# Kernel optimization log

Measured on AMD Instinct MI355X. Metric: run time of the kernel, lower is better.

## Reference

```python
import jax, jax.numpy as jnp
import numpy as np

N, E, B = 50000, 800000, 512
IN, H, OUT = 128, 64, 32
BN_EPS = 1e-5


def setup_inputs() -> dict:
    key = jax.random.key(0)
    ks = jax.random.split(key, 32)
    inp = {}
    inp["x"] = jax.random.normal(ks[0], (N, IN), dtype=jnp.float32)
    inp["edge_index"] = jax.random.randint(ks[1], (2, E), 0, N, dtype=jnp.int64)
    inp["batch"] = jnp.sort(jax.random.randint(ks[2], (N,), 0, B, dtype=jnp.int64))
    inp["batch_size"] = B
    # GINConv MLP params: Linear(cin,H) -> BN(H) -> ReLU -> Linear(H,H)
    cins = [IN, H, H]
    ki = 3
    for i, cin in enumerate(cins):
        inp[f"c{i}_W1"] = jax.random.normal(ks[ki], (cin, H), dtype=jnp.float32) / np.sqrt(cin); ki += 1
        inp[f"c{i}_b1"] = jnp.zeros((H,), jnp.float32)
        inp[f"c{i}_g1"] = jnp.ones((H,), jnp.float32)
        inp[f"c{i}_bt1"] = jnp.zeros((H,), jnp.float32)
        inp[f"c{i}_W2"] = jax.random.normal(ks[ki], (H, H), dtype=jnp.float32) / np.sqrt(H); ki += 1
        inp[f"c{i}_b2"] = jnp.zeros((H,), jnp.float32)
    # final MLP (norm=None): Linear(H,H) -> ReLU -> [dropout, eval: identity] -> Linear(H,OUT)
    inp["f_W1"] = jax.random.normal(ks[ki], (H, H), dtype=jnp.float32) / np.sqrt(H); ki += 1
    inp["f_b1"] = jnp.zeros((H,), jnp.float32)
    inp["f_W2"] = jax.random.normal(ks[ki], (H, OUT), dtype=jnp.float32) / np.sqrt(H)
    inp["f_b2"] = jnp.zeros((OUT,), jnp.float32)
    return inp


def _bn(h, g, bt):
    # BatchNorm1d, training-mode statistics (biased variance), eps=1e-5
    mean = h.mean(axis=0)
    var = ((h - mean) ** 2).mean(axis=0)
    return g * (h - mean) * jax.lax.rsqrt(var + BN_EPS) + bt


def _gin_conv(x, src, dst, W1, b1, g1, bt1, W2, b2):
    # sum-aggregate neighbor features: agg[i] = sum_{(j->i)} x[j]
    agg = jax.ops.segment_sum(x[src], dst, num_segments=N)  # [N,H_in]
    h = x + agg  # (1+eps)*x + agg, eps=0
    h = jax.nn.relu(_bn(h @ W1 + b1, g1, bt1))
    return h @ W2 + b2


def reference(x, edge_index, batch, batch_size,
              c0_W1, c0_b1, c0_g1, c0_bt1, c0_W2, c0_b2,
              c1_W1, c1_b1, c1_g1, c1_bt1, c1_W2, c1_b2,
              c2_W1, c2_b1, c2_g1, c2_bt1, c2_W2, c2_b2,
              f_W1, f_b1, f_W2, f_b2):
    src, dst = edge_index[0], edge_index[1]
    convs = [(c0_W1, c0_b1, c0_g1, c0_bt1, c0_W2, c0_b2),
             (c1_W1, c1_b1, c1_g1, c1_bt1, c1_W2, c1_b2),
             (c2_W1, c2_b1, c2_g1, c2_bt1, c2_W2, c2_b2)]
    for p in convs:
        x = jax.nn.relu(_gin_conv(x, src, dst, *p))
    # global_add_pool over graph ids
    pooled = jax.ops.segment_sum(x, batch, num_segments=batch_size)  # [B,H]
    h = jax.nn.relu(pooled @ f_W1 + f_b1)  # dropout=0.5 skipped (eval mode)
    return h @ f_W2 + f_b2  # [B,OUT]
```

## Files before the change

### kernel.cpp

```cpp
#include <hip/hip_runtime.h>
#include <hip/hip_bf16.h>

#define NN 50000
#define EE 800000
#define BB 512
#define DIN 128
#define HH 64
#define DOUT 32
#define BN_EPS 1e-5f
#define SCAN_BLOCKS 196

template <int CIN>
__global__ __launch_bounds__(256) void proj_kernel(const float* __restrict__ X,
                                                   const float* __restrict__ W,
                                                   float* __restrict__ Q)
{
    __shared__ float sW[CIN * 64];
    __shared__ float sX[16 * CIN];
    const int tid = threadIdx.x;
    const int row0 = blockIdx.x * 16;

    for (int i = tid; i < CIN * 16; i += 256)
        ((float4*)sW)[i] = ((const float4*)W)[i];
    const float* Xb = X + (size_t)row0 * CIN;
    for (int i = tid; i < 16 * CIN / 4; i += 256)
        ((float4*)sX)[i] = ((const float4*)Xb)[i];
    __syncthreads();

    const int col = tid & 63;
    const int r0  = tid >> 6;
    float acc[4] = {0.f, 0.f, 0.f, 0.f};
    for (int k = 0; k < CIN; k += 4) {
        const float w0 = sW[(k + 0) * 64 + col];
        const float w1 = sW[(k + 1) * 64 + col];
        const float w2 = sW[(k + 2) * 64 + col];
        const float w3 = sW[(k + 3) * 64 + col];
#pragma unroll
        for (int rr = 0; rr < 4; ++rr) {
            const float4 xv = *(const float4*)&sX[(r0 + rr * 4) * CIN + k];
            acc[rr] = fmaf(xv.x, w0, acc[rr]);
            acc[rr] = fmaf(xv.y, w1, acc[rr]);
            acc[rr] = fmaf(xv.z, w2, acc[rr]);
            acc[rr] = fmaf(xv.w, w3, acc[rr]);
        }
    }
#pragma unroll
    for (int rr = 0; rr < 4; ++rr) {
        const int row = row0 + r0 + rr * 4;
        Q[(size_t)row * 64 + col] = acc[rr];
    }
}

__global__ __launch_bounds__(256) void hist_kernel(const int* __restrict__ dst,
                                                   int* __restrict__ deg)
{
    const int e = blockIdx.x * 256 + threadIdx.x;
    atomicAdd(&deg[dst[e]], 1);
}

__global__ __launch_bounds__(256) void scanA_kernel(const int* __restrict__ deg,
                                                    int* __restrict__ offs,
                                                    int* __restrict__ blockSums)
{
    __shared__ int s[256];
    const int t = threadIdx.x;
    const int i = blockIdx.x * 256 + t;
    const int v = (i < NN) ? deg[i] : 0;
    s[t] = v;
    __syncthreads();
    for (int off = 1; off < 256; off <<= 1) {
        const int a = (t >= off) ? s[t - off] : 0;
        __syncthreads();
        s[t] += a;
        __syncthreads();
    }
    if (i < NN) offs[i] = s[t] - v;
    if (t == 255) blockSums[blockIdx.x] = s[255];
}

__global__ __launch_bounds__(256) void scanB_kernel(const int* __restrict__ blockSums,
                                                    int* __restrict__ blockOff)
{
    __shared__ int s[256];
    const int t = threadIdx.x;
    const int v = (t < SCAN_BLOCKS) ? blockSums[t] : 0;
    s[t] = v;
    __syncthreads();
    for (int off = 1; off < 256; off <<= 1) {
        const int a = (t >= off) ? s[t - off] : 0;
        __syncthreads();
        s[t] += a;
        __syncthreads();
    }
    if (t < SCAN_BLOCKS) blockOff[t] = s[t] - v;
}

__global__ __launch_bounds__(256) void scanC_kernel(int* __restrict__ offs,
                                                    int* __restrict__ cursor,
                                                    const int* __restrict__ blockOff)
{
    const int i = blockIdx.x * 256 + threadIdx.x;
    if (i < NN) {
        const int o = offs[i] + blockOff[blockIdx.x];
        offs[i] = o;
        cursor[i] = o;
    }
    if (i == 0) offs[NN] = EE;
}

__global__ __launch_bounds__(256) void scatter_kernel(const int* __restrict__ src,
                                                      const int* __restrict__ dst,
                                                      int* __restrict__ cursor,
                                                      int* __restrict__ srcSorted)
{
    const int e = blockIdx.x * 256 + threadIdx.x;
    const int pos = atomicAdd(&cursor[dst[e]], 1);
    srcSorted[pos] = src[e];
}

__global__ __launch_bounds__(256) void gather_kernel(const float* __restrict__ Q,
                                                     const int* __restrict__ offs,
                                                     const int* __restrict__ srcSorted,
                                                     const float* __restrict__ b1,
                                                     float* __restrict__ Z)
{
    const int tid  = threadIdx.x;
    const int col  = tid & 63;
    const int node = blockIdx.x * 4 + (tid >> 6);
    const int o0 = offs[node];
    const int o1 = offs[node + 1];
    float acc = Q[(size_t)node * 64 + col] + b1[col];
    int j = o0;
    for (; j + 4 <= o1; j += 4) {
        const int i0 = srcSorted[j + 0];
        const int i1 = srcSorted[j + 1];
        const int i2 = srcSorted[j + 2];
        const int i3 = srcSorted[j + 3];
        const float a0 = Q[(size_t)i0 * 64 + col];
        const float a1 = Q[(size_t)i1 * 64 + col];
        const float a2 = Q[(size_t)i2 * 64 + col];
        const float a3 = Q[(size_t)i3 * 64 + col];
        acc += a0; acc += a1; acc += a2; acc += a3;
    }
    for (; j < o1; ++j) acc += Q[(size_t)srcSorted[j] * 64 + col];
    Z[(size_t)node * 64 + col] = acc;
}

__global__ __launch_bounds__(256) void stats_kernel(const float* __restrict__ Z,
                                                    float* __restrict__ sums,
                                                    float* __restrict__ sumsq)
{
    const int tid = threadIdx.x;
    const int c4 = tid & 15;
    const int rl = tid >> 4;
    float4 s  = {0.f, 0.f, 0.f, 0.f};
    float4 ss = {0.f, 0.f, 0.f, 0.f};
    const int rowstep = 16 * gridDim.x;
    for (int r = blockIdx.x * 16 + rl; r < NN; r += rowstep) {
        const float4 z = ((const float4*)Z)[(size_t)r * 16 + c4];
        s.x += z.x; s.y += z.y; s.z += z.z; s.w += z.w;
        ss.x += z.x * z.x; ss.y += z.y * z.y; ss.z += z.z * z.z; ss.w += z.w * z.w;
    }
    __shared__ float red[256 * 8];
    float* rp = &red[tid * 8];
    rp[0] = s.x; rp[1] = s.y; rp[2] = s.z; rp[3] = s.w;
    rp[4] = ss.x; rp[5] = ss.y; rp[6] = ss.z; rp[7] = ss.w;
    __syncthreads();
    if (tid < 16) {
        float acc[8] = {0, 0, 0, 0, 0, 0, 0, 0};
        for (int r2 = 0; r2 < 16; ++r2) {
            const float* q2 = &red[(r2 * 16 + tid) * 8];
#pragma unroll
            for (int j = 0; j < 8; ++j) acc[j] += q2[j];
        }
#pragma unroll
        for (int j = 0; j < 4; ++j) {
            atomicAdd(&sums[tid * 4 + j], acc[j]);
            atomicAdd(&sumsq[tid * 4 + j], acc[4 + j]);
        }
    }
}

__global__ void bn_finalize(const float* __restrict__ sums, const float* __restrict__ sumsq,
                            const float* __restrict__ g, const float* __restrict__ bt,
                            float* __restrict__ scale, float* __restrict__ shift)
{
    const int c = threadIdx.x;
    const float inv_n = 1.0f / (float)NN;
    const float mean = sums[c] * inv_n;
    const float var = fmaxf(sumsq[c] * inv_n - mean * mean, 0.f);
    const float sc = g[c] * rsqrtf(var + BN_EPS);
    scale[c] = sc;
    shift[c] = bt[c] - mean * sc;
}

template <bool POOL>
__global__ __launch_bounds__(256) void gemm2_kernel(const float* __restrict__ Z,
                                                    const float* __restrict__ scale,
                                                    const float* __restrict__ shift,
                                                    const float* __restrict__ W2,
                                                    const float* __restrict__ b2,
                                                    const int* __restrict__ batch,
                                                    float* __restrict__ out)
{
    __shared__ float sW[64 * 64];
    __shared__ float sH[16 * 64];
    const int tid = threadIdx.x;
    const int row0 = blockIdx.x * 16;

    for (int i = tid; i < 64 * 16; i += 256)
        ((float4*)sW)[i] = ((const float4*)W2)[i];
    const float4* Zb = (const float4*)(Z + (size_t)row0 * 64);
    for (int i = tid; i < 16 * 16; i += 256) {
        const float4 z = Zb[i];
        const int c4 = i & 15;
        const float4 sc = ((const float4*)scale)[c4];
        const float4 sh = ((const float4*)shift)[c4];
        float4 h;
        h.x = fmaxf(fmaf(z.x, sc.x, sh.x), 0.f);
        h.y = fmaxf(fmaf(z.y, sc.y, sh.y), 0.f);
        h.z = fmaxf(fmaf(z.z, sc.z, sh.z), 0.f);
        h.w = fmaxf(fmaf(z.w, sc.w, sh.w), 0.f);
        ((float4*)sH)[i] = h;
    }
    __syncthreads();

    const int col = tid & 63;
    const int r0  = tid >> 6;
    const float bc = b2[col];
    float acc[4] = {bc, bc, bc, bc};
    for (int k = 0; k < 64; k += 4) {
        const float w0 = sW[(k + 0) * 64 + col];
        const float w1 = sW[(k + 1) * 64 + col];
        const float w2 = sW[(k + 2) * 64 + col];
        const float w3 = sW[(k + 3) * 64 + col];
#pragma unroll
        for (int rr = 0; rr < 4; ++rr) {
            const float4 hv = *(const float4*)&sH[(r0 + rr * 4) * 64 + k];
            acc[rr] = fmaf(hv.x, w0, acc[rr]);
            acc[rr] = fmaf(hv.y, w1, acc[rr]);
            acc[rr] = fmaf(hv.z, w2, acc[rr]);
            acc[rr] = fmaf(hv.w, w3, acc[rr]);
        }
    }
#pragma unroll
    for (int rr = 0; rr < 4; ++rr) {
        const int row = row0 + r0 + rr * 4;
        const float v = fmaxf(acc[rr], 0.f);
        if (POOL) {
            atomicAdd(&out[(size_t)batch[row] * 64 + col], v);
        } else {
            out[(size_t)row * 64 + col] = v;
        }
    }
}

__global__ __launch_bounds__(256) void final_mlp(const float* __restrict__ P,
                                                 const float* __restrict__ W1,
                                                 const float* __restrict__ b1,
                                                 const float* __restrict__ W2,
                                                 const float* __restrict__ b2,
                                                 float* __restrict__ out)
{
    __shared__ float sW1[64 * 64];
    __shared__ float sW2[64 * 32];
    __shared__ float sH[4 * 64];
    const int tid = threadIdx.x;
    const int row0 = blockIdx.x * 4;

    for (int i = tid; i < 1024; i += 256) ((float4*)sW1)[i] = ((const float4*)W1)[i];
    for (int i = tid; i < 512; i += 256) ((float4*)sW2)[i] = ((const float4*)W2)[i];
    __syncthreads();

    const int col = tid & 63;
    const int r = tid >> 6;
    float acc = b1[col];
    const float* prow = P + (size_t)(row0 + r) * 64;
    for (int k = 0; k < 64; ++k) acc = fmaf(prow[k], sW1[k * 64 + col], acc);
    sH[r * 64 + col] = fmaxf(acc, 0.f);
    __syncthreads();

    if (tid < 128) {
        const int c = tid & 31;
        const int r2 = tid >> 5;
        float a2 = b2[c];
        for (int k = 0; k < 64; ++k) a2 = fmaf(sH[r2 * 64 + k], sW2[k * 32 + c], a2);
        out[(size_t)(row0 + r2) * 32 + c] = a2;
    }
}

extern "C" void kernel_launch(void* const* d_in, const int* in_sizes, int n_in,
                              void* d_out, int out_size, void* d_ws, size_t ws_size,
                              hipStream_t stream)
{
    const float* x   = (const float*)d_in[0];
    const int* ei    = (const int*)d_in[1];
    const int* batch = (const int*)d_in[2];
    const float* cW1[3] = {(const float*)d_in[4],  (const float*)d_in[10], (const float*)d_in[16]};
    const float* cb1[3] = {(const float*)d_in[5],  (const float*)d_in[11], (const float*)d_in[17]};
    const float* cg1[3] = {(const float*)d_in[6],  (const float*)d_in[12], (const float*)d_in[18]};
    const float* cbt[3] = {(const float*)d_in[7],  (const float*)d_in[13], (const float*)d_in[19]};
    const float* cW2[3] = {(const float*)d_in[8],  (const float*)d_in[14], (const float*)d_in[20]};
    const float* cb2[3] = {(const float*)d_in[9],  (const float*)d_in[15], (const float*)d_in[21]};
    const float* fW1 = (const float*)d_in[22];
    const float* fb1 = (const float*)d_in[23];
    const float* fW2 = (const float*)d_in[24];
    const float* fb2 = (const float*)d_in[25];
    float* out = (float*)d_out;

    float* bufX   = (float*)d_ws;
    float* q      = bufX + (size_t)NN * 64;
    float* pooled = q + (size_t)NN * 64;
    float* sums   = pooled + (size_t)BB * 64;
    float* sumsq  = sums + 64;
    float* scale  = sumsq + 64;
    float* shift  = scale + 64;
    int* offs      = (int*)(shift + 64);
    int* cursor    = offs + (NN + 1);
    int* blockSums = cursor + (NN + 1);
    int* blockOff  = blockSums + 256;
    int* srcSorted = blockOff + 256;

    const int* esrc = ei;
    const int* edst = ei + EE;

    const int gemm_blocks = NN / 16;
    const int edge_blocks = EE / 256;

    hipMemsetAsync(cursor, 0, (NN + 1) * sizeof(int), stream);
    hist_kernel<<<edge_blocks, 256, 0, stream>>>(edst, cursor);
    scanA_kernel<<<SCAN_BLOCKS, 256, 0, stream>>>(cursor, offs, blockSums);
    scanB_kernel<<<1, 256, 0, stream>>>(blockSums, blockOff);
    scanC_kernel<<<SCAN_BLOCKS, 256, 0, stream>>>(offs, cursor, blockOff);
    scatter_kernel<<<edge_blocks, 256, 0, stream>>>(esrc, edst, cursor, srcSorted);

    for (int layer = 0; layer < 3; ++layer) {
        if (layer == 0)
            proj_kernel<DIN><<<gemm_blocks, 256, 0, stream>>>(x, cW1[0], q);
        else
            proj_kernel<HH><<<gemm_blocks, 256, 0, stream>>>(bufX, cW1[layer], q);

        gather_kernel<<<NN / 4, 256, 0, stream>>>(q, offs, srcSorted, cb1[layer], bufX);

        hipMemsetAsync(sums, 0, 128 * sizeof(float), stream);
        stats_kernel<<<200, 256, 0, stream>>>(bufX, sums, sumsq);

        bn_finalize<<<1, 64, 0, stream>>>(sums, sumsq, cg1[layer], cbt[layer], scale, shift);

        if (layer < 2) {
            gemm2_kernel<false><<<gemm_blocks, 256, 0, stream>>>(bufX, scale, shift, cW2[layer],
                                                                 cb2[layer], nullptr, bufX);
        } else {
            hipMemsetAsync(pooled, 0, (size_t)BB * 64 * sizeof(float), stream);
            gemm2_kernel<true><<<gemm_blocks, 256, 0, stream>>>(bufX, scale, shift, cW2[layer],
                                                                cb2[layer], batch, pooled);
        }
    }

    final_mlp<<<BB / 4, 256, 0, stream>>>(pooled, fW1, fb1, fW2, fb2, out);
}
```

Measured before the change: 408.0 us.

## Store projections in fp16, fuse BN stats into gather, and drop launches

Projection output is now stored as packed half2, which halves the bytes read by the irregular neighbor gather. The gather kernel becomes grid-strided and accumulates BatchNorm sums and sums of squares itself, so the separate stats kernel and its reread of Z go away. BN finalize moves into gemm2, and the memsets are folded into scanC. The CSR build records per-edge ranks during the histogram so the scatter needs no second atomic pass. The fp16 intermediate adds rounding error to the aggregated features, which could affect accuracy tolerance.

Result: no change. 402.8 us (-1.3%).

```diff
diff --git a/kernel.cpp b/kernel.cpp
--- a/kernel.cpp
+++ b/kernel.cpp
@@ -1,5 +1,5 @@
 #include <hip/hip_runtime.h>
-#include <hip/hip_bf16.h>
+#include <hip/hip_fp16.h>
 
 #define NN 50000
 #define EE 800000
@@ -9,11 +9,13 @@
 #define DOUT 32
 #define BN_EPS 1e-5f
 #define SCAN_BLOCKS 196
+#define NGRP 6250
+#define GATHER_GRID 1024
 
 template <int CIN>
 __global__ __launch_bounds__(256) void proj_kernel(const float* __restrict__ X,
                                                    const float* __restrict__ W,
-                                                   float* __restrict__ Q)
+                                                   __half2* __restrict__ Qh)
 {
     __shared__ float sW[CIN * 64];
     __shared__ float sX[16 * CIN];
@@ -27,35 +29,33 @@
         ((float4*)sX)[i] = ((const float4*)Xb)[i];
     __syncthreads();
 
-    const int col = tid & 63;
-    const int r0  = tid >> 6;
-    float acc[4] = {0.f, 0.f, 0.f, 0.f};
-    for (int k = 0; k < CIN; k += 4) {
-        const float w0 = sW[(k + 0) * 64 + col];
-        const float w1 = sW[(k + 1) * 64 + col];
-        const float w2 = sW[(k + 2) * 64 + col];
-        const float w3 = sW[(k + 3) * 64 + col];
-#pragma unroll
-        for (int rr = 0; rr < 4; ++rr) {
-            const float4 xv = *(const float4*)&sX[(r0 + rr * 4) * CIN + k];
-            acc[rr] = fmaf(xv.x, w0, acc[rr]);
-            acc[rr] = fmaf(xv.y, w1, acc[rr]);
-            acc[rr] = fmaf(xv.z, w2, acc[rr]);
-            acc[rr] = fmaf(xv.w, w3, acc[rr]);
-        }
-    }
-#pragma unroll
-    for (int rr = 0; rr < 4; ++rr) {
-        const int row = row0 + r0 + rr * 4;
-        Q[(size_t)row * 64 + col] = acc[rr];
-    }
-}
-
-__global__ __launch_bounds__(256) void hist_kernel(const int* __restrict__ dst,
-                                                   int* __restrict__ deg)
+    const int col2 = tid & 31;
+    const int rg   = tid >> 5;
+    float2 acc0 = {0.f, 0.f};
+    float2 acc1 = {0.f, 0.f};
+    const float* x0p = &sX[(rg * 2 + 0) * CIN];
+    const float* x1p = &sX[(rg * 2 + 1) * CIN];
+#pragma unroll 4
+    for (int k = 0; k < CIN; ++k) {
+        const float2 w = *(const float2*)&sW[k * 64 + col2 * 2];
+        const float x0 = x0p[k];
+        const float x1 = x1p[k];
+        acc0.x = fmaf(x0, w.x, acc0.x);
+        acc0.y = fmaf(x0, w.y, acc0.y);
+        acc1.x = fmaf(x1, w.x, acc1.x);
+        acc1.y = fmaf(x1, w.y, acc1.y);
+    }
+    const int r0 = row0 + rg * 2;
+    Qh[(size_t)(r0 + 0) * 32 + col2] = __floats2half2_rn(acc0.x, acc0.y);
+    Qh[(size_t)(r0 + 1) * 32 + col2] = __floats2half2_rn(acc1.x, acc1.y);
+}
+
+__global__ __launch_bounds__(256) void hist_rank_kernel(const int* __restrict__ dst,
+                                                        int* __restrict__ deg,
+                                                        int* __restrict__ rank)
 {
     const int e = blockIdx.x * 256 + threadIdx.x;
-    atomicAdd(&deg[dst[e]], 1);
+    rank[e] = atomicAdd(&deg[dst[e]], 1);
 }
 
 __global__ __launch_bounds__(256) void scanA_kernel(const int* __restrict__ deg,
@@ -96,108 +96,101 @@
 }
 
 __global__ __launch_bounds__(256) void scanC_kernel(int* __restrict__ offs,
-                                                    int* __restrict__ cursor,
-                                                    const int* __restrict__ blockOff)
+                                                    const int* __restrict__ blockOff,
+                                                    float* __restrict__ statsbuf,
+                                                    float* __restrict__ pooled)
 {
     const int i = blockIdx.x * 256 + threadIdx.x;
-    if (i < NN) {
-        const int o = offs[i] + blockOff[blockIdx.x];
-        offs[i] = o;
-        cursor[i] = o;
-    }
+    if (i < NN) offs[i] += blockOff[blockIdx.x];
     if (i == 0) offs[NN] = EE;
+    if (i < 384) statsbuf[i] = 0.f;
+    if (i < BB * 64) pooled[i] = 0.f;
 }
 
 __global__ __launch_bounds__(256) void scatter_kernel(const int* __restrict__ src,
                                                       const int* __restrict__ dst,
-                                                      int* __restrict__ cursor,
+                                                      const int* __restrict__ rank,
+                                                      const int* __restrict__ offs,
                                                       int* __restrict__ srcSorted)
 {
     const int e = blockIdx.x * 256 + threadIdx.x;
-    const int pos = atomicAdd(&cursor[dst[e]], 1);
+    const int pos = offs[dst[e]] + rank[e];
     srcSorted[pos] = src[e];
 }
 
-__global__ __launch_bounds__(256) void gather_kernel(const float* __restrict__ Q,
+__global__ __launch_bounds__(256) void gather_kernel(const __half2* __restrict__ Qh,
                                                      const int* __restrict__ offs,
                                                      const int* __restrict__ srcSorted,
                                                      const float* __restrict__ b1,
-                                                     float* __restrict__ Z)
+                                                     float* __restrict__ Z,
+                                                     float* __restrict__ sums,
+                                                     float* __restrict__ sumsq)
 {
     const int tid  = threadIdx.x;
-    const int col  = tid & 63;
-    const int node = blockIdx.x * 4 + (tid >> 6);
-    const int o0 = offs[node];
-    const int o1 = offs[node + 1];
-    float acc = Q[(size_t)node * 64 + col] + b1[col];
-    int j = o0;
-    for (; j + 4 <= o1; j += 4) {
-        const int i0 = srcSorted[j + 0];
-        const int i1 = srcSorted[j + 1];
-        const int i2 = srcSorted[j + 2];
-        const int i3 = srcSorted[j + 3];
-        const float a0 = Q[(size_t)i0 * 64 + col];
-        const float a1 = Q[(size_t)i1 * 64 + col];
-        const float a2 = Q[(size_t)i2 * 64 + col];
-        const float a3 = Q[(size_t)i3 * 64 + col];
-        acc += a0; acc += a1; acc += a2; acc += a3;
-    }
-    for (; j < o1; ++j) acc += Q[(size_t)srcSorted[j] * 64 + col];
-    Z[(size_t)node * 64 + col] = acc;
-}
-
-__global__ __launch_bounds__(256) void stats_kernel(const float* __restrict__ Z,
-                                                    float* __restrict__ sums,
-                                                    float* __restrict__ sumsq)
-{
-    const int tid = threadIdx.x;
-    const int c4 = tid & 15;
-    const int rl = tid >> 4;
-    float4 s  = {0.f, 0.f, 0.f, 0.f};
-    float4 ss = {0.f, 0.f, 0.f, 0.f};
-    const int rowstep = 16 * gridDim.x;
-    for (int r = blockIdx.x * 16 + rl; r < NN; r += rowstep) {
-        const float4 z = ((const float4*)Z)[(size_t)r * 16 + c4];
-        s.x += z.x; s.y += z.y; s.z += z.z; s.w += z.w;
-        ss.x += z.x * z.x; ss.y += z.y * z.y; ss.z += z.z * z.z; ss.w += z.w * z.w;
-    }
-    __shared__ float red[256 * 8];
-    float* rp = &red[tid * 8];
-    rp[0] = s.x; rp[1] = s.y; rp[2] = s.z; rp[3] = s.w;
-    rp[4] = ss.x; rp[5] = ss.y; rp[6] = ss.z; rp[7] = ss.w;
-    __syncthreads();
-    if (tid < 16) {
-        float acc[8] = {0, 0, 0, 0, 0, 0, 0, 0};
-        for (int r2 = 0; r2 < 16; ++r2) {
-            const float* q2 = &red[(r2 * 16 + tid) * 8];
+    const int half = tid & 31;
+    const int sel8 = tid >> 5;
+    const float2 bb = ((const float2*)b1)[half];
+    float2 s  = {0.f, 0.f};
+    float2 ss = {0.f, 0.f};
+
+    for (int g = blockIdx.x; g < NGRP; g += GATHER_GRID) {
+        const int node = g * 8 + sel8;
+        const int o0 = offs[node];
+        const int o1 = offs[node + 1];
+        float2 acc = __half22float2(Qh[(size_t)node * 32 + half]);
+        acc.x += bb.x;
+        acc.y += bb.y;
+        int j = o0;
+        for (; j + 4 <= o1; j += 4) {
+            const int i0 = srcSorted[j + 0];
+            const int i1 = srcSorted[j + 1];
+            const int i2 = srcSorted[j + 2];
+            const int i3 = srcSorted[j + 3];
+            const float2 a0 = __half22float2(Qh[(size_t)i0 * 32 + half]);
+            const float2 a1 = __half22float2(Qh[(size_t)i1 * 32 + half]);
+            const float2 a2 = __half22float2(Qh[(size_t)i2 * 32 + half]);
+            const float2 a3 = __half22float2(Qh[(size_t)i3 * 32 + half]);
+            acc.x += a0.x + a1.x + a2.x + a3.x;
+            acc.y += a0.y + a1.y + a2.y + a3.y;
+        }
+        for (; j < o1; ++j) {
+            const float2 a = __half22float2(Qh[(size_t)srcSorted[j] * 32 + half]);
+            acc.x += a.x;
+            acc.y += a.y;
+        }
+        ((float2*)Z)[(size_t)node * 32 + half] = acc;
+        s.x += acc.x; s.y += acc.y;
+        ss.x += acc.x * acc.x; ss.y += acc.y * acc.y;
+    }
+
+    __shared__ float red[8][32][4];
+    red[sel8][half][0] = s.x;
+    red[sel8][half][1] = s.y;
+    red[sel8][half][2] = ss.x;
+    red[sel8][half][3] = ss.y;
+    __syncthreads();
+    if (tid < 32) {
+        float a0 = 0.f, a1 = 0.f, a2 = 0.f, a3 = 0.f;
 #pragma unroll
-            for (int j = 0; j < 8; ++j) acc[j] += q2[j];
-        }
-#pragma unroll
-        for (int j = 0; j < 4; ++j) {
-            atomicAdd(&sums[tid * 4 + j], acc[j]);
-            atomicAdd(&sumsq[tid * 4 + j], acc[4 + j]);
-        }
-    }
-}
-
-__global__ void bn_finalize(const float* __restrict__ sums, const float* __restrict__ sumsq,
-                            const float* __restrict__ g, const float* __restrict__ bt,
-                            float* __restrict__ scale, float* __restrict__ shift)
-{
-    const int c = threadIdx.x;
-    const float inv_n = 1.0f / (float)NN;
-    const float mean = sums[c] * inv_n;
-    const float var = fmaxf(sumsq[c] * inv_n - mean * mean, 0.f);
-    const float sc = g[c] * rsqrtf(var + BN_EPS);
-    scale[c] = sc;
-    shift[c] = bt[c] - mean * sc;
+        for (int r = 0; r < 8; ++r) {
+            a0 += red[r][tid][0];
+            a1 += red[r][tid][1];
+            a2 += red[r][tid][2];
+            a3 += red[r][tid][3];
+        }
+        atomicAdd(&sums[2 * tid + 0], a0);
+        atomicAdd(&sums[2 * tid + 1], a1);
+        atomicAdd(&sumsq[2 * tid + 0], a2);
+        atomicAdd(&sumsq[2 * tid + 1], a3);
+    }
 }
 
 template <bool POOL>
 __global__ __launch_bounds__(256) void gemm2_kernel(const float* __restrict__ Z,
-                                                    const float* __restrict__ scale,
-                                                    const float* __restrict__ shift,
+                                                    const float* __restrict__ sums,
+                                                    const float* __restrict__ sumsq,
+                                                    const float* __restrict__ g1,
+                                                    const float* __restrict__ bt1,
                                                     const float* __restrict__ W2,
                                                     const float* __restrict__ b2,
                                                     const int* __restrict__ batch,
@@ -205,17 +198,30 @@
 {
     __shared__ float sW[64 * 64];
     __shared__ float sH[16 * 64];
+    __shared__ float sScale[64];
+    __shared__ float sShift[64];
     const int tid = threadIdx.x;
     const int row0 = blockIdx.x * 16;
 
+    if (tid < 64) {
+        const float inv_n = 1.0f / (float)NN;
+        const float mean = sums[tid] * inv_n;
+        const float var = fmaxf(sumsq[tid] * inv_n - mean * mean, 0.f);
+        const float sc = g1[tid] * rsqrtf(var + BN_EPS);
+        sScale[tid] = sc;
+        sShift[tid] = bt1[tid] - mean * sc;
+    }
     for (int i = tid; i < 64 * 16; i += 256)
         ((float4*)sW)[i] = ((const float4*)W2)[i];
+    __syncthreads();
+
     const float4* Zb = (const float4*)(Z + (size_t)row0 * 64);
-    for (int i = tid; i < 16 * 16; i += 256) {
+    {
+        const int i = tid;
         const float4 z = Zb[i];
         const int c4 = i & 15;
-        const float4 sc = ((const float4*)scale)[c4];
-        const float4 sh = ((const float4*)shift)[c4];
+        const float4 sc = ((const float4*)sScale)[c4];
+        const float4 sh = ((const float4*)sShift)[c4];
         float4 h;
         h.x = fmaxf(fmaf(z.x, sc.x, sh.x), 0.f);
         h.y = fmaxf(fmaf(z.y, sc.y, sh.y), 0.f);
@@ -308,18 +314,16 @@
     const float* fb2 = (const float*)d_in[25];
     float* out = (float*)d_out;
 
-    float* bufX   = (float*)d_ws;
-    float* q      = bufX + (size_t)NN * 64;
-    float* pooled = q + (size_t)NN * 64;
-    float* sums   = pooled + (size_t)BB * 64;
-    float* sumsq  = sums + 64;
-    float* scale  = sumsq + 64;
-    float* shift  = scale + 64;
-    int* offs      = (int*)(shift + 64);
-    int* cursor    = offs + (NN + 1);
-    int* blockSums = cursor + (NN + 1);
-    int* blockOff  = blockSums + 256;
-    int* srcSorted = blockOff + 256;
+    float* bufX     = (float*)d_ws;
+    __half2* Qh     = (__half2*)(bufX + (size_t)NN * 64);
+    float* pooled   = (float*)(Qh + (size_t)NN * 32);
+    float* statsbuf = pooled + (size_t)BB * 64;
+    int* deg        = (int*)(statsbuf + 384);
+    int* offs       = deg + NN;
+    int* rank       = offs + (NN + 1);
+    int* blockSums  = rank + EE;
+    int* blockOff   = blockSums + 256;
+    int* srcSorted  = blockOff + 256;
 
     const int* esrc = ei;
     const int* edst = ei + EE;
@@ -327,33 +331,33 @@
     const int gemm_blocks = NN / 16;
     const int edge_blocks = EE / 256;
 
-    hipMemsetAsync(cursor, 0, (NN + 1) * sizeof(int), stream);
-    hist_kernel<<<edge_blocks, 256, 0, stream>>>(edst, cursor);
-    scanA_kernel<<<SCAN_BLOCKS, 256, 0, stream>>>(cursor, offs, blockSums);
+    hipMemsetAsync(deg, 0, NN * sizeof(int), stream);
+    hist_rank_kernel<<<edge_blocks, 256, 0, stream>>>(edst, deg, rank);
+    scanA_kernel<<<SCAN_BLOCKS, 256, 0, stream>>>(deg, offs, blockSums);
     scanB_kernel<<<1, 256, 0, stream>>>(blockSums, blockOff);
-    scanC_kernel<<<SCAN_BLOCKS, 256, 0, stream>>>(offs, cursor, blockOff);
-    scatter_kernel<<<edge_blocks, 256, 0, stream>>>(esrc, edst, cursor, srcSorted);
+    scanC_kernel<<<SCAN_BLOCKS, 256, 0, stream>>>(offs, blockOff, statsbuf, pooled);
+    scatter_kernel<<<edge_blocks, 256, 0, stream>>>(esrc, edst, rank, offs, srcSorted);
 
     for (int layer = 0; layer < 3; ++layer) {
+        float* sums  = statsbuf + layer * 128;
+        float* sumsq = sums + 64;
+
         if (layer == 0)
-            proj_kernel<DIN><<<gemm_blocks, 256, 0, stream>>>(x, cW1[0], q);
+            proj_kernel<DIN><<<gemm_blocks, 256, 0, stream>>>(x, cW1[0], Qh);
         else
-            proj_kernel<HH><<<gemm_blocks, 256, 0, stream>>>(bufX, cW1[layer], q);
-
-        gather_kernel<<<NN / 4, 256, 0, stream>>>(q, offs, srcSorted, cb1[layer], bufX);
-
-        hipMemsetAsync(sums, 0, 128 * sizeof(float), stream);
-        stats_kernel<<<200, 256, 0, stream>>>(bufX, sums, sumsq);
-
-        bn_finalize<<<1, 64, 0, stream>>>(sums, sumsq, cg1[layer], cbt[layer], scale, shift);
+            proj_kernel<HH><<<gemm_blocks, 256, 0, stream>>>(bufX, cW1[layer], Qh);
+
+        gather_kernel<<<GATHER_GRID, 256, 0, stream>>>(Qh, offs, srcSorted, cb1[layer],
+                                                       bufX, sums, sumsq);
 
         if (layer < 2) {
-            gemm2_kernel<false><<<gemm_blocks, 256, 0, stream>>>(bufX, scale, shift, cW2[layer],
-                                                                 cb2[layer], nullptr, bufX);
+            gemm2_kernel<false><<<gemm_blocks, 256, 0, stream>>>(bufX, sums, sumsq, cg1[layer],
+                                                                 cbt[layer], cW2[layer], cb2[layer],
+                                                                 nullptr, bufX);
         } else {
-            hipMemsetAsync(pooled, 0, (size_t)BB * 64 * sizeof(float), stream);
-            gemm2_kernel<true><<<gemm_blocks, 256, 0, stream>>>(bufX, scale, shift, cW2[layer],
-                                                                cb2[layer], batch, pooled);
+            gemm2_kernel<true><<<gemm_blocks, 256, 0, stream>>>(bufX, sums, sumsq, cg1[layer],
+                                                                cbt[layer], cW2[layer], cb2[layer],
+                                                                batch, pooled);
         }
     }
 
```
